# Kernel tuning notes

Measured on AMD Instinct MI355X. Metric: run time of the kernel, lower is better.

## Reference

```python
import jax, jax.numpy as jnp
import numpy as np

V = 4096          # total nodes (pedestrian + group)
F = 64            # input feature dim
H = 16            # hidden dim
CTX = 4           # context (phi) dim
P = 3072          # num_ped_nodes
G = 1024          # group conflict matrix size
EPS = 1e-8
SLOPE = 0.2


def setup_inputs() -> dict:
    key = jax.random.key(0)
    ks = jax.random.split(key, 8)
    node_features = jax.random.normal(ks[0], (V, F), dtype=jnp.float32)
    a = jax.random.uniform(ks[1], (V, V), dtype=jnp.float32)
    adjacency = jnp.where(a > 0.9, a, 0.0)
    node_positions = jax.random.normal(ks[2], (V, 2), dtype=jnp.float32) * 10.0
    node_velocities = jax.random.normal(ks[3], (V, 2), dtype=jnp.float32)
    node_types = jax.random.randint(ks[4], (V,), 0, 2, dtype=jnp.int64)
    conflict_softmax_group = jax.random.uniform(ks[5], (G, G), dtype=jnp.float32)
    W_proj = jax.random.normal(ks[6], (F, H), dtype=jnp.float32) * 0.1
    w_score = jax.random.normal(ks[7], (2 * H + CTX,), dtype=jnp.float32) * 0.1
    return {
        "node_features": node_features,
        "adjacency": adjacency,
        "node_positions": node_positions,
        "node_velocities": node_velocities,
        "node_types": node_types,
        "num_ped_nodes": P,
        "conflict_softmax_group": conflict_softmax_group,
        "W_proj": W_proj,
        "w_score": w_score,
    }


def reference(node_features, adjacency, node_positions, node_velocities,
              node_types, num_ped_nodes, conflict_softmax_group, W_proj, w_score):
    v = node_features.shape[0]
    hdim = W_proj.shape[1]

    h = node_features @ W_proj  # [V, H]

    # --- phi = [dist, vel_diff, dir_align, norm_conf] : [V, V, 4] ---
    dpos = node_positions[:, None, :] - node_positions[None, :, :]   # [V,V,2]
    dist = jnp.linalg.norm(dpos, axis=-1)                            # [V,V]
    dvel = node_velocities[:, None, :] - node_velocities[None, :, :]
    vel_diff = jnp.linalg.norm(dvel, axis=-1)
    speed = jnp.linalg.norm(node_velocities, axis=-1, keepdims=True)
    dirv = node_velocities / (speed + EPS)                           # [V,2]
    dir_align = jnp.clip(dirv @ dirv.T, -1.0, 1.0)                   # [V,V]

    # vectorized replacement of the Python double-loop scatter:
    g = jnp.arange(v) - num_ped_nodes
    gsize = conflict_softmax_group.shape[0]
    valid = (node_types == 1) & (g >= 0) & (g < gsize)               # [V]
    gc = jnp.clip(g, 0, gsize - 1)
    norm_conf = jnp.where(valid[:, None] & valid[None, :],
                          conflict_softmax_group[gc[:, None], gc[None, :]], 0.0)

    phi = jnp.stack([dist, vel_diff, dir_align, norm_conf], axis=-1)  # [V,V,4]

    # --- attention score: concat([h_i, h_j, phi]) @ w_score, decomposed to
    # avoid materializing the [V,V,2H+4] pair tensor (same math) ---
    li = h @ w_score[:hdim]             # [V]  contribution of h_i
    lj = h @ w_score[hdim:2 * hdim]     # [V]  contribution of h_j
    logits = li[:, None] + lj[None, :] + phi @ w_score[2 * hdim:]    # [V,V]
    logits = jnp.where(logits >= 0, logits, SLOPE * logits)          # LeakyReLU

    suppress = jnp.where(adjacency > 0, 0.0, -1e9)
    attn = jax.nn.softmax(logits + suppress, axis=1)
    attn = attn * adjacency
    attn = attn / (attn.sum(axis=1, keepdims=True) + EPS)
    attended = attn @ h                 # [V, H]
    return attended, attn, phi
```

## Files before the change

kernel.cpp:

```cpp
#include <hip/hip_runtime.h>

#define V 4096
#define F 64
#define H 16
#define GSZ 1024
#define EPS 1e-8f
#define SLOPE 0.2f
#define NITER (V / 256)

typedef float f4 __attribute__((ext_vector_type(4)));

__global__ __launch_bounds__(256) void prep_kernel(
    const float* __restrict__ feat,
    const float* __restrict__ pos,
    const float* __restrict__ vel,
    const int*   __restrict__ types,
    const int*   __restrict__ nped,
    const float* __restrict__ Wp,
    const float* __restrict__ wscore,
    f4*    __restrict__ hg,
    float* __restrict__ li,
    f4*    __restrict__ na,
    f4*    __restrict__ nb)
{
    int i = blockIdx.x * blockDim.x + threadIdx.x;
    if (i >= V) return;

    float acc[H];
#pragma unroll
    for (int c = 0; c < H; ++c) acc[c] = 0.f;
    for (int f = 0; f < F; ++f) {
        float x = feat[i * F + f];
#pragma unroll
        for (int c = 0; c < H; ++c) acc[c] += x * Wp[f * H + c];
    }
    float sli = 0.f, slj = 0.f;
#pragma unroll
    for (int c = 0; c < H; ++c) {
        sli += acc[c] * wscore[c];
        slj += acc[c] * wscore[H + c];
    }
#pragma unroll
    for (int c4 = 0; c4 < H / 4; ++c4) {
        f4 hv;
        hv.x = acc[c4 * 4 + 0];
        hv.y = acc[c4 * 4 + 1];
        hv.z = acc[c4 * 4 + 2];
        hv.w = acc[c4 * 4 + 3];
        hg[c4 * V + i] = hv;
    }
    li[i] = sli;

    float vx = vel[i * 2], vy = vel[i * 2 + 1];
    float inv = 1.f / (sqrtf(vx * vx + vy * vy) + EPS);
    int P = nped[0];
    int g = i - P;
    int gc = (types[i] == 1 && g >= 0 && g < GSZ) ? g : -1;

    f4 A, B;
    A.x = pos[i * 2]; A.y = pos[i * 2 + 1]; A.z = vx; A.w = vy;
    B.x = vx * inv;   B.y = vy * inv;       B.z = slj; B.w = __int_as_float(gc);
    na[i] = A;
    nb[i] = B;
}

__global__ __launch_bounds__(256, 8) void row_kernel(
    const float* __restrict__ adj,
    const float* __restrict__ conflict,
    const float* __restrict__ wscore,
    const f4*    __restrict__ hg,
    const float* __restrict__ li,
    const f4*    __restrict__ na,
    const f4*    __restrict__ nb,
    float* __restrict__ out_att,
    float* __restrict__ out_attn,
    float* __restrict__ out_phi)
{
    const int i   = blockIdx.x;
    const int tid = threadIdx.x;

    __shared__ float red[8];
    __shared__ float atile[4 * H];

    const f4 ra = na[i];
    const f4 rb = nb[i];
    const float pix = ra.x, piy = ra.y, vix = ra.z, viy = ra.w;
    const float dix = rb.x, diy = rb.y;
    const int   gi  = __float_as_int(rb.w);
    const float li_i = li[i];
    const float w0 = wscore[2 * H + 0];
    const float w1 = wscore[2 * H + 1];
    const float w2 = wscore[2 * H + 2];
    const float w3 = wscore[2 * H + 3];

    const float* adjrow  = adj + (size_t)i * V;
    f4*          phirow  = (f4*)out_phi + (size_t)i * V;
    float*       attnrow = out_attn + (size_t)i * V;

    float ea[NITER];
    float s = 0.f, t = 0.f;
#pragma unroll
    for (int k = 0; k < NITER; ++k) {
        int j = tid + k * 256;
        float a = adjrow[j];
        f4 A = na[j];
        f4 B = nb[j];
        float dx = pix - A.x, dy = piy - A.y;
        float dist = sqrtf(dx * dx + dy * dy);
        float dvx = vix - A.z, dvy = viy - A.w;
        float vdiff = sqrtf(dvx * dvx + dvy * dvy);
        float al = fminf(1.f, fmaxf(-1.f, dix * B.x + diy * B.y));
        int gj = __float_as_int(B.w);
        float conf = (gi >= 0 && gj >= 0) ? conflict[(size_t)gi * GSZ + gj] : 0.f;

        f4 ph;
        ph.x = dist; ph.y = vdiff; ph.z = al; ph.w = conf;
        __builtin_nontemporal_store(ph, phirow + j);

        float lg = li_i + B.z + dist * w0 + vdiff * w1 + al * w2 + conf * w3;
        lg = (lg >= 0.f) ? lg : SLOPE * lg;
        float e = (a > 0.f) ? __expf(fminf(lg, 80.f)) : 0.f;
        ea[k] = e * a;
        s += e;
        t += e * a;
    }
#pragma unroll
    for (int off = 32; off; off >>= 1) {
        s += __shfl_xor(s, off);
        t += __shfl_xor(t, off);
    }
    if ((tid & 63) == 0) { red[tid >> 6] = s; red[4 + (tid >> 6)] = t; }
    __syncthreads();
    s = red[0] + red[1] + red[2] + red[3];
    t = red[4] + red[5] + red[6] + red[7];
    const float denom = t + EPS * s;
    const float dinv  = (denom > 0.f) ? 1.f / denom : 0.f;

    float acc[H];
#pragma unroll
    for (int c = 0; c < H; ++c) acc[c] = 0.f;
#pragma unroll
    for (int k = 0; k < NITER; ++k) {
        int j = tid + k * 256;
        float w = ea[k] * dinv;
        __builtin_nontemporal_store(w, attnrow + j);
#pragma unroll
        for (int c4 = 0; c4 < H / 4; ++c4) {
            f4 hv = hg[c4 * V + j];
            acc[c4 * 4 + 0] += w * hv.x;
            acc[c4 * 4 + 1] += w * hv.y;
            acc[c4 * 4 + 2] += w * hv.z;
            acc[c4 * 4 + 3] += w * hv.w;
        }
    }
#pragma unroll
    for (int c = 0; c < H; ++c)
#pragma unroll
        for (int off = 32; off; off >>= 1) acc[c] += __shfl_xor(acc[c], off);

    if ((tid & 63) == 0) {
        int wv = tid >> 6;
#pragma unroll
        for (int c = 0; c < H; ++c) atile[wv * H + c] = acc[c];
    }
    __syncthreads();
    if (tid < H) {
        out_att[(size_t)i * H + tid] =
            atile[tid] + atile[H + tid] + atile[2 * H + tid] + atile[3 * H + tid];
    }
}

extern "C" void kernel_launch(void* const* d_in, const int* in_sizes, int n_in,
                              void* d_out, int out_size, void* d_ws, size_t ws_size,
                              hipStream_t stream) {
    const float* feat     = (const float*)d_in[0];
    const float* adj      = (const float*)d_in[1];
    const float* pos      = (const float*)d_in[2];
    const float* vel      = (const float*)d_in[3];
    const int*   types    = (const int*)  d_in[4];
    const int*   nped     = (const int*)  d_in[5];
    const float* conflict = (const float*)d_in[6];
    const float* Wp       = (const float*)d_in[7];
    const float* wscore   = (const float*)d_in[8];

    float* out = (float*)d_out;
    float* out_att  = out;
    float* out_attn = out + (size_t)V * H;
    float* out_phi  = out + (size_t)V * H + (size_t)V * V;

    float* ws = (float*)d_ws;
    f4*    hg = (f4*)ws;
    float* li = ws + (size_t)V * H;
    f4*    na = (f4*)(li + V);
    f4*    nb = na + V;

    prep_kernel<<<dim3(V / 256), dim3(256), 0, stream>>>(
        feat, pos, vel, types, nped, Wp, wscore, hg, li, na, nb);

    row_kernel<<<dim3(V), dim3(256), 0, stream>>>(
        adj, conflict, wscore, hg, li, na, nb, out_att, out_attn, out_phi);
}
```

Measured before the change: 92.84 us.

## Process two rows per block and store h as packed bf16

Each block of the row kernel now handles two output rows. The per-column node data (na, nb, h) is loaded once and reused for both rows. The hidden features h are rounded to bf16 and packed into two uint4 arrays per node, which halves the bytes read in the aggregation loop. This trades register pressure (launch bounds lowered from 8 to 4) and some precision in attended for fewer redundant loads, although the kernel is likely dominated by the phi and attn output writes.

```diff
diff --git a/kernel.cpp b/kernel.cpp
--- a/kernel.cpp
+++ b/kernel.cpp
@@ -7,8 +7,18 @@
 #define EPS 1e-8f
 #define SLOPE 0.2f
 #define NITER (V / 256)
+#define R 2
 
 typedef float f4 __attribute__((ext_vector_type(4)));
+typedef unsigned int u32;
+
+__device__ __forceinline__ u32 pack_bf16(float x, float y) {
+    u32 bx = __float_as_uint(x);
+    u32 by = __float_as_uint(y);
+    bx += 0x7fffu + ((bx >> 16) & 1u);
+    by += 0x7fffu + ((by >> 16) & 1u);
+    return (bx >> 16) | (by & 0xffff0000u);
+}
 
 __global__ __launch_bounds__(256) void prep_kernel(
     const float* __restrict__ feat,
@@ -18,7 +28,8 @@
     const int*   __restrict__ nped,
     const float* __restrict__ Wp,
     const float* __restrict__ wscore,
-    f4*    __restrict__ hg,
+    uint4* __restrict__ hgA,
+    uint4* __restrict__ hgB,
     float* __restrict__ li,
     f4*    __restrict__ na,
     f4*    __restrict__ nb)
@@ -40,15 +51,13 @@
         sli += acc[c] * wscore[c];
         slj += acc[c] * wscore[H + c];
     }
-#pragma unroll
-    for (int c4 = 0; c4 < H / 4; ++c4) {
-        f4 hv;
-        hv.x = acc[c4 * 4 + 0];
-        hv.y = acc[c4 * 4 + 1];
-        hv.z = acc[c4 * 4 + 2];
-        hv.w = acc[c4 * 4 + 3];
-        hg[c4 * V + i] = hv;
-    }
+    uint4 wa, wb;
+    wa.x = pack_bf16(acc[0], acc[1]);  wa.y = pack_bf16(acc[2], acc[3]);
+    wa.z = pack_bf16(acc[4], acc[5]);  wa.w = pack_bf16(acc[6], acc[7]);
+    wb.x = pack_bf16(acc[8], acc[9]);  wb.y = pack_bf16(acc[10], acc[11]);
+    wb.z = pack_bf16(acc[12], acc[13]); wb.w = pack_bf16(acc[14], acc[15]);
+    hgA[i] = wa;
+    hgB[i] = wb;
     li[i] = sli;
 
     float vx = vel[i * 2], vy = vel[i * 2 + 1];
@@ -64,11 +73,12 @@
     nb[i] = B;
 }
 
-__global__ __launch_bounds__(256, 8) void row_kernel(
+__global__ __launch_bounds__(256, 4) void row_kernel(
     const float* __restrict__ adj,
     const float* __restrict__ conflict,
     const float* __restrict__ wscore,
-    const f4*    __restrict__ hg,
+    const uint4* __restrict__ hgA,
+    const uint4* __restrict__ hgB,
     const float* __restrict__ li,
     const f4*    __restrict__ na,
     const f4*    __restrict__ nb,
@@ -76,97 +86,131 @@
     float* __restrict__ out_attn,
     float* __restrict__ out_phi)
 {
-    const int i   = blockIdx.x;
+    const int i0  = blockIdx.x * R;
     const int tid = threadIdx.x;
 
-    __shared__ float red[8];
-    __shared__ float atile[4 * H];
-
-    const f4 ra = na[i];
-    const f4 rb = nb[i];
-    const float pix = ra.x, piy = ra.y, vix = ra.z, viy = ra.w;
-    const float dix = rb.x, diy = rb.y;
-    const int   gi  = __float_as_int(rb.w);
-    const float li_i = li[i];
+    __shared__ float red_s[4][R];
+    __shared__ float red_t[4][R];
+    __shared__ float atile[4][R * H];
+
+    float pix[R], piy[R], vix[R], viy[R], dix[R], diy[R], lii[R];
+    int   gi[R];
+#pragma unroll
+    for (int r = 0; r < R; ++r) {
+        f4 ra = na[i0 + r];
+        f4 rb = nb[i0 + r];
+        pix[r] = ra.x; piy[r] = ra.y; vix[r] = ra.z; viy[r] = ra.w;
+        dix[r] = rb.x; diy[r] = rb.y;
+        gi[r]  = __float_as_int(rb.w);
+        lii[r] = li[i0 + r];
+    }
     const float w0 = wscore[2 * H + 0];
     const float w1 = wscore[2 * H + 1];
     const float w2 = wscore[2 * H + 2];
     const float w3 = wscore[2 * H + 3];
 
-    const float* adjrow  = adj + (size_t)i * V;
-    f4*          phirow  = (f4*)out_phi + (size_t)i * V;
-    float*       attnrow = out_attn + (size_t)i * V;
-
-    float ea[NITER];
-    float s = 0.f, t = 0.f;
+    float ea[R][NITER];
+    float s[R], t[R];
+#pragma unroll
+    for (int r = 0; r < R; ++r) { s[r] = 0.f; t[r] = 0.f; }
+
 #pragma unroll
     for (int k = 0; k < NITER; ++k) {
-        int j = tid + k * 256;
-        float a = adjrow[j];
+        const int j = tid + k * 256;
         f4 A = na[j];
         f4 B = nb[j];
-        float dx = pix - A.x, dy = piy - A.y;
-        float dist = sqrtf(dx * dx + dy * dy);
-        float dvx = vix - A.z, dvy = viy - A.w;
-        float vdiff = sqrtf(dvx * dvx + dvy * dvy);
-        float al = fminf(1.f, fmaxf(-1.f, dix * B.x + diy * B.y));
-        int gj = __float_as_int(B.w);
-        float conf = (gi >= 0 && gj >= 0) ? conflict[(size_t)gi * GSZ + gj] : 0.f;
-
-        f4 ph;
-        ph.x = dist; ph.y = vdiff; ph.z = al; ph.w = conf;
-        __builtin_nontemporal_store(ph, phirow + j);
-
-        float lg = li_i + B.z + dist * w0 + vdiff * w1 + al * w2 + conf * w3;
-        lg = (lg >= 0.f) ? lg : SLOPE * lg;
-        float e = (a > 0.f) ? __expf(fminf(lg, 80.f)) : 0.f;
-        ea[k] = e * a;
-        s += e;
-        t += e * a;
-    }
-#pragma unroll
-    for (int off = 32; off; off >>= 1) {
-        s += __shfl_xor(s, off);
-        t += __shfl_xor(t, off);
-    }
-    if ((tid & 63) == 0) { red[tid >> 6] = s; red[4 + (tid >> 6)] = t; }
-    __syncthreads();
-    s = red[0] + red[1] + red[2] + red[3];
-    t = red[4] + red[5] + red[6] + red[7];
-    const float denom = t + EPS * s;
-    const float dinv  = (denom > 0.f) ? 1.f / denom : 0.f;
-
-    float acc[H];
-#pragma unroll
-    for (int c = 0; c < H; ++c) acc[c] = 0.f;
-#pragma unroll
-    for (int k = 0; k < NITER; ++k) {
-        int j = tid + k * 256;
-        float w = ea[k] * dinv;
-        __builtin_nontemporal_store(w, attnrow + j);
-#pragma unroll
-        for (int c4 = 0; c4 < H / 4; ++c4) {
-            f4 hv = hg[c4 * V + j];
-            acc[c4 * 4 + 0] += w * hv.x;
-            acc[c4 * 4 + 1] += w * hv.y;
-            acc[c4 * 4 + 2] += w * hv.z;
-            acc[c4 * 4 + 3] += w * hv.w;
+        const int gj = __float_as_int(B.w);
+#pragma unroll
+        for (int r = 0; r < R; ++r) {
+            float a = adj[(size_t)(i0 + r) * V + j];
+            float dx = pix[r] - A.x, dy = piy[r] - A.y;
+            float dist = sqrtf(dx * dx + dy * dy);
+            float dvx = vix[r] - A.z, dvy = viy[r] - A.w;
+            float vdiff = sqrtf(dvx * dvx + dvy * dvy);
+            float al = fminf(1.f, fmaxf(-1.f, dix[r] * B.x + diy[r] * B.y));
+            float conf = (gi[r] >= 0 && gj >= 0) ? conflict[(size_t)gi[r] * GSZ + gj] : 0.f;
+
+            f4 ph;
+            ph.x = dist; ph.y = vdiff; ph.z = al; ph.w = conf;
+            __builtin_nontemporal_store(ph, (f4*)out_phi + (size_t)(i0 + r) * V + j);
+
+            float lg = lii[r] + B.z + dist * w0 + vdiff * w1 + al * w2 + conf * w3;
+            lg = (lg >= 0.f) ? lg : SLOPE * lg;
+            float e = (a > 0.f) ? __expf(fminf(lg, 80.f)) : 0.f;
+            ea[r][k] = e * a;
+            s[r] += e;
+            t[r] += e * a;
         }
     }
 #pragma unroll
-    for (int c = 0; c < H; ++c)
-#pragma unroll
-        for (int off = 32; off; off >>= 1) acc[c] += __shfl_xor(acc[c], off);
-
+    for (int r = 0; r < R; ++r) {
+#pragma unroll
+        for (int off = 32; off; off >>= 1) {
+            s[r] += __shfl_xor(s[r], off);
+            t[r] += __shfl_xor(t[r], off);
+        }
+    }
     if ((tid & 63) == 0) {
         int wv = tid >> 6;
 #pragma unroll
-        for (int c = 0; c < H; ++c) atile[wv * H + c] = acc[c];
+        for (int r = 0; r < R; ++r) { red_s[wv][r] = s[r]; red_t[wv][r] = t[r]; }
     }
     __syncthreads();
-    if (tid < H) {
-        out_att[(size_t)i * H + tid] =
-            atile[tid] + atile[H + tid] + atile[2 * H + tid] + atile[3 * H + tid];
+    float dinv[R];
+#pragma unroll
+    for (int r = 0; r < R; ++r) {
+        float ss = red_s[0][r] + red_s[1][r] + red_s[2][r] + red_s[3][r];
+        float tt = red_t[0][r] + red_t[1][r] + red_t[2][r] + red_t[3][r];
+        float denom = tt + EPS * ss;
+        dinv[r] = (denom > 0.f) ? 1.f / denom : 0.f;
+    }
+
+    float acc[R][H];
+#pragma unroll
+    for (int r = 0; r < R; ++r)
+#pragma unroll
+        for (int c = 0; c < H; ++c) acc[r][c] = 0.f;
+
+#pragma unroll
+    for (int k = 0; k < NITER; ++k) {
+        const int j = tid + k * 256;
+        uint4 wa = hgA[j];
+        uint4 wb = hgB[j];
+        float hv[H];
+        hv[0]  = __uint_as_float(wa.x << 16); hv[1]  = __uint_as_float(wa.x & 0xffff0000u);
+        hv[2]  = __uint_as_float(wa.y << 16); hv[3]  = __uint_as_float(wa.y & 0xffff0000u);
+        hv[4]  = __uint_as_float(wa.z << 16); hv[5]  = __uint_as_float(wa.z & 0xffff0000u);
+        hv[6]  = __uint_as_float(wa.w << 16); hv[7]  = __uint_as_float(wa.w & 0xffff0000u);
+        hv[8]  = __uint_as_float(wb.x << 16); hv[9]  = __uint_as_float(wb.x & 0xffff0000u);
+        hv[10] = __uint_as_float(wb.y << 16); hv[11] = __uint_as_float(wb.y & 0xffff0000u);
+        hv[12] = __uint_as_float(wb.z << 16); hv[13] = __uint_as_float(wb.z & 0xffff0000u);
+        hv[14] = __uint_as_float(wb.w << 16); hv[15] = __uint_as_float(wb.w & 0xffff0000u);
+#pragma unroll
+        for (int r = 0; r < R; ++r) {
+            float w = ea[r][k] * dinv[r];
+            __builtin_nontemporal_store(w, out_attn + (size_t)(i0 + r) * V + j);
+#pragma unroll
+            for (int c = 0; c < H; ++c) acc[r][c] += w * hv[c];
+        }
+    }
+#pragma unroll
+    for (int r = 0; r < R; ++r)
+#pragma unroll
+        for (int c = 0; c < H; ++c)
+#pragma unroll
+            for (int off = 32; off; off >>= 1) acc[r][c] += __shfl_xor(acc[r][c], off);
+
+    if ((tid & 63) == 0) {
+        int wv = tid >> 6;
+#pragma unroll
+        for (int r = 0; r < R; ++r)
+#pragma unroll
+            for (int c = 0; c < H; ++c) atile[wv][r * H + c] = acc[r][c];
+    }
+    __syncthreads();
+    if (tid < R * H) {
+        out_att[(size_t)i0 * H + tid] =
+            atile[0][tid] + atile[1][tid] + atile[2][tid] + atile[3][tid];
     }
 }
 
@@ -189,14 +233,15 @@
     float* out_phi  = out + (size_t)V * H + (size_t)V * V;
 
     float* ws = (float*)d_ws;
-    f4*    hg = (f4*)ws;
-    float* li = ws + (size_t)V * H;
-    f4*    na = (f4*)(li + V);
-    f4*    nb = na + V;
+    uint4* hgA = (uint4*)ws;
+    uint4* hgB = hgA + V;
+    float* li  = (float*)(hgB + V);
+    f4*    na  = (f4*)(li + V);
+    f4*    nb  = na + V;
 
     prep_kernel<<<dim3(V / 256), dim3(256), 0, stream>>>(
-        feat, pos, vel, types, nped, Wp, wscore, hg, li, na, nb);
-
-    row_kernel<<<dim3(V), dim3(256), 0, stream>>>(
-        adj, conflict, wscore, hg, li, na, nb, out_att, out_attn, out_phi);
-}
+        feat, pos, vel, types, nped, Wp, wscore, hgA, hgB, li, na, nb);
+
+    row_kernel<<<dim3(V / R), dim3(256), 0, stream>>>(
+        adj, conflict, wscore, hgA, hgB, li, na, nb, out_att, out_attn, out_phi);
+}
```

Measured after the change: 172.7 us. 86.0% more time.
